# Optimization experiments

Hardware: AMD Instinct MI355X
Metric: run time of the kernel (lower is better)

Reference implementation:

```python
import jax, jax.numpy as jnp
import numpy as np

HEADS, LEVELS, POINTS, ZANCH = 8, 4, 8, 4
EMBED = 256
SHAPES = np.array([[92, 160], [46, 80], [23, 40], [12, 20]], dtype=np.int32)


def setup_inputs() -> dict:
    key = jax.random.key(0)
    k = jax.random.split(key, 9)
    bs, nq = 1, 10000
    nv = int((SHAPES[:, 0].astype(np.int64) * SHAPES[:, 1]).sum())  # 19560
    f32 = jnp.float32
    return dict(
        query=jax.random.normal(k[0], (bs, nq, EMBED), f32),
        value=jax.random.normal(k[1], (bs, nv, EMBED), f32),
        query_pos=0.1 * jax.random.normal(k[2], (bs, nq, EMBED), f32),
        reference_points=jax.random.uniform(k[3], (bs, nq, ZANCH, 2), dtype=f32),
        spatial_shapes=jnp.asarray(SHAPES),
        W_off=0.01 * jax.random.normal(k[4], (EMBED, HEADS * LEVELS * POINTS * 2), f32),
        b_off=0.5 * jax.random.normal(k[5], (HEADS * LEVELS * POINTS * 2,), f32),
        W_attn=0.01 * jax.random.normal(k[6], (EMBED, HEADS * LEVELS * POINTS), f32),
        b_attn=jnp.zeros((HEADS * LEVELS * POINTS,), f32),
        W_val=(1.0 / np.sqrt(EMBED)) * jax.random.normal(k[7], (EMBED, EMBED), f32),
        b_val=jnp.zeros((EMBED,), f32),
        W_out=(1.0 / np.sqrt(EMBED)) * jax.random.normal(k[8], (EMBED, EMBED), f32),
        b_out=jnp.zeros((EMBED,), f32),
    )


def _bilinear(v_l, x, y, Hl, Wl):
    # v_l: [bs, heads, Hl*Wl, d]; x, y: [bs, nq, heads, P] pixel coords
    # (torch grid_sample, align_corners=False, zero padding): px = loc*W - 0.5
    bs, nq, heads, P = x.shape
    d = v_l.shape[-1]
    x0 = jnp.floor(x)
    y0 = jnp.floor(y)
    lx = x - x0
    ly = y - y0
    x0i = x0.astype(jnp.int32)
    y0i = y0.astype(jnp.int32)

    def corner(xi, yi, w):
        valid = (xi >= 0) & (xi < Wl) & (yi >= 0) & (yi < Hl)
        idx = jnp.clip(yi, 0, Hl - 1) * Wl + jnp.clip(xi, 0, Wl - 1)
        idxr = idx.transpose(0, 2, 1, 3).reshape(bs, heads, nq * P)
        g = jnp.take_along_axis(v_l, idxr[..., None], axis=2)  # [bs,heads,nq*P,d]
        g = g.reshape(bs, heads, nq, P, d).transpose(0, 2, 1, 3, 4)
        return g * (w * valid.astype(w.dtype))[..., None]

    return (corner(x0i, y0i, (1 - lx) * (1 - ly))
            + corner(x0i + 1, y0i, lx * (1 - ly))
            + corner(x0i, y0i + 1, (1 - lx) * ly)
            + corner(x0i + 1, y0i + 1, lx * ly))


def reference(query, value, query_pos, reference_points, spatial_shapes,
              W_off, b_off, W_attn, b_attn, W_val, b_val, W_out, b_out):
    shapes = np.asarray(spatial_shapes)  # static per-level (H, W)
    bs, nq, E = query.shape
    heads = HEADS
    L = shapes.shape[0]
    P = W_off.shape[1] // (heads * L * 2)
    Z = reference_points.shape[2]
    d = E // heads

    residual = query
    q = query + query_pos
    v = (value @ W_val + b_val).reshape(bs, -1, heads, d)

    off = (q @ W_off + b_off).reshape(bs, nq, heads, L, P, 2)
    attn = jax.nn.softmax((q @ W_attn + b_attn).reshape(bs, nq, heads, L * P), axis=-1)
    attn = attn.reshape(bs, nq, heads, L, P)

    # normalize offsets by (W, H) per level, add Z-anchor reference points
    norm = jnp.asarray(np.stack([shapes[:, 1], shapes[:, 0]], -1), off.dtype)  # [L,2]
    off = off / norm[None, None, None, :, None, :]
    loc = (reference_points[:, :, None, None, None, :, :]
           + off.reshape(bs, nq, heads, L, P // Z, Z, 2)).reshape(bs, nq, heads, L, P, 2)

    starts = np.concatenate([[0], np.cumsum(shapes[:, 0].astype(np.int64) * shapes[:, 1])])
    out = jnp.zeros((bs, nq, heads, d), q.dtype)
    for l in range(L):  # small fixed loop over pyramid levels
        Hl, Wl = int(shapes[l, 0]), int(shapes[l, 1])
        v_l = v[:, int(starts[l]):int(starts[l + 1])].transpose(0, 2, 1, 3)  # [bs,heads,HW,d]
        x = loc[:, :, :, l, :, 0] * Wl - 0.5
        y = loc[:, :, :, l, :, 1] * Hl - 0.5
        sampled = _bilinear(v_l, x, y, Hl, Wl)  # [bs,nq,heads,P,d]
        out = out + (sampled * attn[:, :, :, l, :, None]).sum(axis=3)

    out = out.reshape(bs, nq, E) @ W_out + b_out
    return out + residual  # dropout is identity at eval
```

## Files before the change

### kernel.cpp

```cpp
#include <hip/hip_runtime.h>
#include <hip/hip_bf16.h>
#include <math.h>

typedef __hip_bfloat16 bf16;
typedef short short8_t __attribute__((ext_vector_type(8)));
typedef float f32x4 __attribute__((ext_vector_type(4)));

#define EMBED 256
#define ZANCH 4

__global__ __launch_bounds__(256) void k_prep(
    const float* __restrict__ Woff, const float* __restrict__ Wattn,
    const float* __restrict__ Wval, const float* __restrict__ Wout,
    bf16* __restrict__ wt,
    const float* __restrict__ value, bf16* __restrict__ vb,
    const float* __restrict__ query, const float* __restrict__ query_pos,
    bf16* __restrict__ qb)
{
    const int b = blockIdx.x;
    const int tid = threadIdx.x;
    if (b < 320) {
        __shared__ float tile[32][33];
        const int tn = b >> 3, tk = b & 7;
        const int r = tid >> 5, c = tid & 31;
        const int n0 = tn * 32, k0t = tk * 32;
#pragma unroll
        for (int rr = r; rr < 32; rr += 8) {
            const int k = k0t + rr;
            const int n = n0 + c;
            float val;
            if (n < 512)       val = Woff[(size_t)k * 512 + n];
            else if (n < 768)  val = Wattn[(size_t)k * 256 + (n - 512)];
            else if (n < 1024) val = Wval[(size_t)k * 256 + (n - 768)];
            else               val = Wout[(size_t)k * 256 + (n - 1024)];
            tile[rr][c] = val;
        }
        __syncthreads();
#pragma unroll
        for (int rr = r; rr < 32; rr += 8) {
            const int n = n0 + rr;
            const int k = k0t + c;
            wt[(size_t)n * 256 + k] = __float2bfloat16(tile[c][rr]);
        }
    } else if (b < 5210) {
        size_t i = ((size_t)(b - 320) * 256 + tid) * 4;
        float4 a = *(const float4*)(value + i);
        vb[i + 0] = __float2bfloat16(a.x);
        vb[i + 1] = __float2bfloat16(a.y);
        vb[i + 2] = __float2bfloat16(a.z);
        vb[i + 3] = __float2bfloat16(a.w);
    } else {
        size_t i = ((size_t)(b - 5210) * 256 + tid) * 4;
        float4 a = *(const float4*)(query + i);
        float4 p = *(const float4*)(query_pos + i);
        qb[i + 0] = __float2bfloat16(a.x + p.x);
        qb[i + 1] = __float2bfloat16(a.y + p.y);
        qb[i + 2] = __float2bfloat16(a.z + p.z);
        qb[i + 3] = __float2bfloat16(a.w + p.w);
    }
}

__global__ __launch_bounds__(256) void k_gemm_vp(
    const bf16* __restrict__ vb, const bf16* __restrict__ Btv,
    const float* __restrict__ bv, bf16* __restrict__ vhl, int Mv,
    const bf16* __restrict__ qb, const bf16* __restrict__ Btcat,
    const float* __restrict__ boff, const float* __restrict__ battn,
    float* __restrict__ raw, int Mq)
{
    __shared__ char sm[33792];
    float* smE  = (float*)sm;
    bf16*  smEv = (bf16*)sm;

    const int tid  = threadIdx.x;
    const int lane = tid & 63;
    const int wv   = tid >> 6;
    const int c16  = lane & 15, quad = lane >> 4;
    const int nwave = wv * 64;

    const bool isval = (blockIdx.y == 3);
    const int M = isval ? Mv : Mq;
    if ((int)blockIdx.x >= (M + 31) / 32) return;
    const int row0 = blockIdx.x * 32;
    const bf16* A  = isval ? vb : qb;
    const bf16* Bt = isval ? Btv : (Btcat + (size_t)(blockIdx.y * 256) * 256);

    f32x4 acc[2][4] = {};
    {
        size_t aoff[2], boffr[4];
#pragma unroll
        for (int mt = 0; mt < 2; ++mt) {
            int r = row0 + mt * 16 + c16;
            r = (r < M) ? r : (M - 1);
            aoff[mt] = (size_t)r * 256 + quad * 8;
        }
#pragma unroll
        for (int nt = 0; nt < 4; ++nt)
            boffr[nt] = (size_t)(nwave + nt * 16 + c16) * 256 + quad * 8;
#pragma unroll
        for (int k0 = 0; k0 < 256; k0 += 32) {
            short8_t a[2], b[4];
#pragma unroll
            for (int mt = 0; mt < 2; ++mt) a[mt] = *(const short8_t*)(A + aoff[mt] + k0);
#pragma unroll
            for (int nt = 0; nt < 4; ++nt) b[nt] = *(const short8_t*)(Bt + boffr[nt] + k0);
#pragma unroll
            for (int mt = 0; mt < 2; ++mt)
#pragma unroll
                for (int nt = 0; nt < 4; ++nt)
                    acc[mt][nt] = __builtin_amdgcn_mfma_f32_16x16x32_bf16(
                        a[mt], b[nt], acc[mt][nt], 0, 0, 0);
        }
    }

    if (isval) {
#pragma unroll
        for (int nt = 0; nt < 4; ++nt) {
            const int colg = nwave + nt * 16 + c16;
            const float bias = bv[colg];
#pragma unroll
            for (int mt = 0; mt < 2; ++mt)
#pragma unroll
                for (int reg = 0; reg < 4; ++reg) {
                    const int rl = mt * 16 + quad * 4 + reg;
                    smEv[rl * 264 + colg] = __float2bfloat16(acc[mt][nt][reg] + bias);
                }
        }
        __syncthreads();
#pragma unroll
        for (int sub = 0; sub < 2; ++sub) {
            const int h = wv * 2 + sub;
            bf16* dsth = vhl + (size_t)h * Mv * 32;
#pragma unroll
            for (int j = 0; j < 2; ++j) {
                const int s = j * 64 + lane;
                const int pix = s >> 2, seg = s & 3;
                const int rg = row0 + pix;
                if (rg < Mv)
                    *(short8_t*)(dsth + (size_t)rg * 32 + seg * 8) =
                        *(const short8_t*)(smEv + pix * 264 + h * 32 + seg * 8);
            }
        }
    } else {
#pragma unroll
        for (int nt = 0; nt < 4; ++nt) {
            const int colg = nwave + nt * 16 + c16;
            const int cg = blockIdx.y * 256 + colg;
            const float bias = (cg < 512) ? boff[cg] : battn[cg - 512];
#pragma unroll
            for (int mt = 0; mt < 2; ++mt)
#pragma unroll
                for (int reg = 0; reg < 4; ++reg) {
                    const int rl = mt * 16 + quad * 4 + reg;
                    smE[rl * 260 + colg] = acc[mt][nt][reg] + bias;
                }
        }
        __syncthreads();
#pragma unroll
        for (int rr = 0; rr < 8; ++rr) {
            const int rl = wv * 8 + rr;
            const int rg = row0 + rl;
            if (rg < Mq)
                *(f32x4*)(raw + (size_t)rg * 768 + blockIdx.y * 256 + lane * 4) =
                    *(const f32x4*)(smE + rl * 260 + lane * 4);
        }
    }
}

__global__ __launch_bounds__(256) void k_sample(
    const bf16* __restrict__ vhl, const float* __restrict__ raw,
    const float* __restrict__ refpts, bf16* __restrict__ outa, int nq, int nv)
{
    __shared__ int   sidx[2][4][256];
    __shared__ float swt[2][4][256];
    const int tid = threadIdx.x;
    const int q0 = blockIdx.x * 2;

    {
        const int l = (tid >> 3) & 3;
        const int p = tid & 7;
        const int z = p & (ZANCH - 1);
        const float Wlf = (l == 0) ? 160.f : (l == 1) ? 80.f : (l == 2) ? 40.f : 20.f;
        const float Hlf = (l == 0) ? 92.f : (l == 1) ? 46.f : (l == 2) ? 23.f : 12.f;
        const int Wli = (l == 0) ? 160 : (l == 1) ? 80 : (l == 2) ? 40 : 20;
        const int Hli = (l == 0) ? 92 : (l == 1) ? 46 : (l == 2) ? 23 : 12;
        const int Stl = (l == 0) ? 0 : (l == 1) ? 14720 : (l == 2) ? 18400 : 19320;

#pragma unroll
        for (int r = 0; r < 2; ++r) {
            const int q = q0 + r;
            const float ox = raw[(size_t)q * 768 + 2 * tid];
            const float oy = raw[(size_t)q * 768 + 2 * tid + 1];
            const float lg = raw[(size_t)q * 768 + 512 + tid];

            float m = lg;
            for (int o = 16; o > 0; o >>= 1) m = fmaxf(m, __shfl_xor(m, o, 32));
            float e = __expf(lg - m);
            float s = e;
            for (int o = 16; o > 0; o >>= 1) s += __shfl_xor(s, o, 32);
            const float aw = e / s;

            const float refx = refpts[(size_t)q * 8 + z * 2 + 0];
            const float refy = refpts[(size_t)q * 8 + z * 2 + 1];
            const float px = refx * Wlf + ox - 0.5f;
            const float py = refy * Hlf + oy - 0.5f;

            const float x0f = floorf(px), y0f = floorf(py);
            const int x0 = (int)x0f, y0 = (int)y0f;
            const float lx = px - x0f, ly = py - y0f;
            const float cw[4] = { (1.f - lx) * (1.f - ly), lx * (1.f - ly),
                                  (1.f - lx) * ly,         lx * ly };
#pragma unroll
            for (int c = 0; c < 4; ++c) {
                const int xi = x0 + (c & 1);
                const int yi = y0 + (c >> 1);
                const bool valid = (xi >= 0) && (xi < Wli) && (yi >= 0) && (yi < Hli);
                const int xc = min(max(xi, 0), Wli - 1);
                const int yc = min(max(yi, 0), Hli - 1);
                sidx[r][c][tid] = Stl + yc * Wli + xc;
                swt[r][c][tid]  = valid ? (cw[c] * aw) : 0.f;
            }
        }
    }
    __syncthreads();

    const int qsel = tid >> 7;
    const int slot = tid & 127;
    const int h = slot >> 4;
    const int cp = slot & 15;
    const int e0 = h * 32;
    const bf16* vbase = vhl + (size_t)h * nv * 32 + cp * 2;

    float acc0 = 0.f, acc1 = 0.f;
#pragma unroll 2
    for (int bb = 0; bb < 128; bb += 16) {
        int   ix[16];
        float wvv[16];
#pragma unroll
        for (int j = 0; j < 16; ++j) {
            const int i = bb + j;
            const int c = i & 3, lp = i >> 2;
            ix[j] = sidx[qsel][c][e0 + lp];
            wvv[j] = swt[qsel][c][e0 + lp];
        }
        int dv[16];
#pragma unroll
        for (int j = 0; j < 16; ++j)
            dv[j] = *(const int*)(vbase + (size_t)ix[j] * 32);
#pragma unroll
        for (int j = 0; j < 16; ++j) {
            acc0 = fmaf(wvv[j], __int_as_float(dv[j] << 16), acc0);
            acc1 = fmaf(wvv[j], __int_as_float(dv[j] & 0xFFFF0000), acc1);
        }
    }
    __hip_bfloat162 o2;
    o2.x = __float2bfloat16(acc0);
    o2.y = __float2bfloat16(acc1);
    *(__hip_bfloat162*)(outa + (size_t)(q0 + qsel) * 256 + h * 32 + cp * 2) = o2;
}

__global__ __launch_bounds__(256) void k_gemm_out(
    const bf16* __restrict__ outa, const bf16* __restrict__ Bto,
    const float* __restrict__ bo, const float* __restrict__ query,
    float* __restrict__ out, int M)
{
    const int row0 = blockIdx.x * 32;
    const int nwave = (threadIdx.x >> 6) * 64;
    const int lane = threadIdx.x & 63;
    const int c16 = lane & 15, quad = lane >> 4;

    f32x4 acc[2][4] = {};
    {
        size_t aoff[2], boffr[4];
#pragma unroll
        for (int mt = 0; mt < 2; ++mt) {
            int r = row0 + mt * 16 + c16;
            r = (r < M) ? r : (M - 1);
            aoff[mt] = (size_t)r * 256 + quad * 8;
        }
#pragma unroll
        for (int nt = 0; nt < 4; ++nt)
            boffr[nt] = (size_t)(nwave + nt * 16 + c16) * 256 + quad * 8;
#pragma unroll
        for (int k0 = 0; k0 < 256; k0 += 32) {
            short8_t a[2], b[4];
#pragma unroll
            for (int mt = 0; mt < 2; ++mt) a[mt] = *(const short8_t*)(outa + aoff[mt] + k0);
#pragma unroll
            for (int nt = 0; nt < 4; ++nt) b[nt] = *(const short8_t*)(Bto + boffr[nt] + k0);
#pragma unroll
            for (int mt = 0; mt < 2; ++mt)
#pragma unroll
                for (int nt = 0; nt < 4; ++nt)
                    acc[mt][nt] = __builtin_amdgcn_mfma_f32_16x16x32_bf16(
                        a[mt], b[nt], acc[mt][nt], 0, 0, 0);
        }
    }
#pragma unroll
    for (int nt = 0; nt < 4; ++nt) {
        int colg = nwave + nt * 16 + c16;
        float bias = bo[colg];
#pragma unroll
        for (int mt = 0; mt < 2; ++mt)
#pragma unroll
            for (int reg = 0; reg < 4; ++reg) {
                int row = row0 + mt * 16 + quad * 4 + reg;
                if (row < M) {
                    size_t o_ = (size_t)row * 256 + colg;
                    float fv = acc[mt][nt][reg] + bias + query[o_];
                    if (!(fv == fv) || fabsf(fv) > 1e30f) fv = 0.f;
                    out[o_] = fv;
                }
            }
    }
}

extern "C" void kernel_launch(void* const* d_in, const int* in_sizes, int n_in,
                              void* d_out, int out_size, void* d_ws, size_t ws_size,
                              hipStream_t stream)
{
    const float* query     = (const float*)d_in[0];
    const float* value     = (const float*)d_in[1];
    const float* query_pos = (const float*)d_in[2];
    const float* refpts    = (const float*)d_in[3];
    const float* Woff  = (const float*)d_in[5];
    const float* boff  = (const float*)d_in[6];
    const float* Wattn = (const float*)d_in[7];
    const float* battn = (const float*)d_in[8];
    const float* Wval  = (const float*)d_in[9];
    const float* bval  = (const float*)d_in[10];
    const float* Wout  = (const float*)d_in[11];
    const float* bout  = (const float*)d_in[12];
    float* out = (float*)d_out;

    const int nq = in_sizes[0] / EMBED;
    const int nv = in_sizes[1] / EMBED;

    char* base = (char*)d_ws;
    bf16*  wt   = (bf16*)base;
    bf16*  qb   = (bf16*)(base + 655360);
    bf16*  vb   = (bf16*)(base + 5775360);
    float* raw  = (float*)(base + 15790080);
    bf16*  outa = (bf16*)(base + 46510080);
    bf16*  vhl  = (bf16*)(base + 51630080);
    const bf16* Btcat = wt;
    const bf16* Btv   = wt + 768 * 256;
    const bf16* Bto   = wt + 1024 * 256;

    k_prep<<<7710, 256, 0, stream>>>(Woff, Wattn, Wval, Wout, wt,
                                     value, vb, query, query_pos, qb);
    k_gemm_vp<<<dim3((nv + 31) / 32, 4), 256, 0, stream>>>(vb, Btv, bval, vhl, nv,
                                                           qb, Btcat, boff, battn, raw, nq);
    k_sample<<<nq / 2, 256, 0, stream>>>(vhl, raw, refpts, outa, nq, nv);
    k_gemm_out<<<(nq + 31) / 32, 256, 0, stream>>>(outa, Bto, bout, query, out, nq);
}
```

Before: 215.4 us.

## Regroup sampling blocks by head pair over eight queries with packed index-weight smem

Each sampling block now covers 8 queries for 2 heads instead of 2 queries for all 8 heads. Block indices are interleaved so that neighbouring blocks touch the same head planes of the value tensor, which should improve cache locality for the gathers. Sample indices and weights are packed into a single int2 shared array, so each sample takes one LDS load instead of two. The grid size stays at 5000 blocks. The softmax still reduces over 32 lanes per head, so it remains correct.

```diff
diff --git a/kernel.cpp b/kernel.cpp
--- a/kernel.cpp
+++ b/kernel.cpp
@@ -170,14 +170,17 @@
     const bf16* __restrict__ vhl, const float* __restrict__ raw,
     const float* __restrict__ refpts, bf16* __restrict__ outa, int nq, int nv)
 {
-    __shared__ int   sidx[2][4][256];
-    __shared__ float swt[2][4][256];
+    __shared__ int2 spr[16][128];
     const int tid = threadIdx.x;
-    const int q0 = blockIdx.x * 2;
+    const int b = blockIdx.x;
+    const int hp = (b & 7) >> 1;
+    const int qg = ((b >> 3) << 1) + (b & 1);
+    const int q0 = qg * 8;
 
     {
-        const int l = (tid >> 3) & 3;
-        const int p = tid & 7;
+        const int lp = tid & 31;
+        const int l = lp >> 3;
+        const int p = lp & 7;
         const int z = p & (ZANCH - 1);
         const float Wlf = (l == 0) ? 160.f : (l == 1) ? 80.f : (l == 2) ? 40.f : 20.f;
         const float Hlf = (l == 0) ? 92.f : (l == 1) ? 46.f : (l == 2) ? 23.f : 12.f;
@@ -187,10 +190,14 @@
 
 #pragma unroll
         for (int r = 0; r < 2; ++r) {
-            const int q = q0 + r;
-            const float ox = raw[(size_t)q * 768 + 2 * tid];
-            const float oy = raw[(size_t)q * 768 + 2 * tid + 1];
-            const float lg = raw[(size_t)q * 768 + 512 + tid];
+            const int g = r * 8 + (tid >> 5);
+            const int q = q0 + (g >> 1);
+            const int head = hp * 2 + (g & 1);
+            const int col = head * 32 + lp;
+
+            const float ox = raw[(size_t)q * 768 + 2 * col];
+            const float oy = raw[(size_t)q * 768 + 2 * col + 1];
+            const float lg = raw[(size_t)q * 768 + 512 + col];
 
             float m = lg;
             for (int o = 16; o > 0; o >>= 1) m = fmaxf(m, __shfl_xor(m, o, 32));
@@ -216,46 +223,40 @@
                 const bool valid = (xi >= 0) && (xi < Wli) && (yi >= 0) && (yi < Hli);
                 const int xc = min(max(xi, 0), Wli - 1);
                 const int yc = min(max(yi, 0), Hli - 1);
-                sidx[r][c][tid] = Stl + yc * Wli + xc;
-                swt[r][c][tid]  = valid ? (cw[c] * aw) : 0.f;
+                const float w = valid ? (cw[c] * aw) : 0.f;
+                spr[g][c * 32 + lp] = make_int2(Stl + yc * Wli + xc, __float_as_int(w));
             }
         }
     }
     __syncthreads();
 
-    const int qsel = tid >> 7;
-    const int slot = tid & 127;
-    const int h = slot >> 4;
-    const int cp = slot & 15;
-    const int e0 = h * 32;
-    const bf16* vbase = vhl + (size_t)h * nv * 32 + cp * 2;
+    const int qs = tid >> 5;
+    const int hh = (tid >> 4) & 1;
+    const int cp = tid & 15;
+    const int g2 = qs * 2 + hh;
+    const bf16* vbase = vhl + (size_t)(hp * 2 + hh) * nv * 32 + cp * 2;
 
     float acc0 = 0.f, acc1 = 0.f;
 #pragma unroll 2
     for (int bb = 0; bb < 128; bb += 16) {
-        int   ix[16];
-        float wvv[16];
+        int2 pr[16];
+#pragma unroll
+        for (int j = 0; j < 16; ++j) pr[j] = spr[g2][bb + j];
+        int dv[16];
+#pragma unroll
+        for (int j = 0; j < 16; ++j)
+            dv[j] = *(const int*)(vbase + (size_t)pr[j].x * 32);
 #pragma unroll
         for (int j = 0; j < 16; ++j) {
-            const int i = bb + j;
-            const int c = i & 3, lp = i >> 2;
-            ix[j] = sidx[qsel][c][e0 + lp];
-            wvv[j] = swt[qsel][c][e0 + lp];
-        }
-        int dv[16];
-#pragma unroll
-        for (int j = 0; j < 16; ++j)
-            dv[j] = *(const int*)(vbase + (size_t)ix[j] * 32);
-#pragma unroll
-        for (int j = 0; j < 16; ++j) {
-            acc0 = fmaf(wvv[j], __int_as_float(dv[j] << 16), acc0);
-            acc1 = fmaf(wvv[j], __int_as_float(dv[j] & 0xFFFF0000), acc1);
+            const float w = __int_as_float(pr[j].y);
+            acc0 = fmaf(w, __int_as_float(dv[j] << 16), acc0);
+            acc1 = fmaf(w, __int_as_float(dv[j] & 0xFFFF0000), acc1);
         }
     }
     __hip_bfloat162 o2;
     o2.x = __float2bfloat16(acc0);
     o2.y = __float2bfloat16(acc1);
-    *(__hip_bfloat162*)(outa + (size_t)(q0 + qsel) * 256 + h * 32 + cp * 2) = o2;
+    *(__hip_bfloat162*)(outa + (size_t)(q0 + qs) * 256 + (hp * 2 + hh) * 32 + cp * 2) = o2;
 }
 
 __global__ __launch_bounds__(256) void k_gemm_out(
@@ -350,6 +351,6 @@
                                      value, vb, query, query_pos, qb);
     k_gemm_vp<<<dim3((nv + 31) / 32, 4), 256, 0, stream>>>(vb, Btv, bval, vhl, nv,
                                                            qb, Btcat, boff, battn, raw, nq);
-    k_sample<<<nq / 2, 256, 0, stream>>>(vhl, raw, refpts, outa, nq, nv);
+    k_sample<<<(nq / 8) * 4, 256, 0, stream>>>(vhl, raw, refpts, outa, nq, nv);
     k_gemm_out<<<(nq + 31) / 32, 256, 0, stream>>>(outa, Bto, bout, query, out, nq);
 }
```

New measurement: 208.9 us. -3.0%, faster.
